# Optimization experiments

Measured on AMD Instinct MI355X. Metric: run time of the kernel, lower is better.

Reference implementation:

```python
import jax, jax.numpy as jnp
import numpy as np
import math

B, S, H, HKV, DH = 2, 2048, 32, 1, 128  # batch, seq, q heads, kv heads, per-head/model dim
D_K = 128


def setup_inputs() -> dict:
    key = jax.random.key(0)
    ks = jax.random.split(key, 11)
    sc = 0.02
    return {
        "query": jax.random.normal(ks[0], (B, S, DH), jnp.float32),
        "key": jax.random.normal(ks[1], (B, S, DH), jnp.float32),
        "values": jax.random.normal(ks[2], (B, S, DH), jnp.float32),
        "W_q": jax.random.normal(ks[3], (DH, H * DH), jnp.float32) * sc,
        "b_q": jnp.zeros((H * DH,), jnp.float32),
        "W_k": jax.random.normal(ks[4], (DH, HKV * DH), jnp.float32) * sc,
        "b_k": jnp.zeros((HKV * DH,), jnp.float32),
        "W_v": jax.random.normal(ks[5], (DH, HKV * DH), jnp.float32) * sc,
        "b_v": jnp.zeros((HKV * DH,), jnp.float32),
        "W_o": jax.random.normal(ks[6], (H * DH, DH), jnp.float32) * sc,
        "b_o": jnp.zeros((DH,), jnp.float32),
    }


def reference(query, key, values, W_q, b_q, W_k, b_k, W_v, b_v, W_o, b_o):
    # Projections (note: the original uses raw .view(-1, H, S, DH), which we
    # replicate exactly — it is a reshape, not a transpose).
    q = (query @ W_q + b_q).reshape(-1, H, S, DH)      # [B,H,S,DH]
    k = (key @ W_k + b_k).reshape(-1, HKV, S, DH)       # [B,1,S,DH]
    v = (values @ W_v + b_v).reshape(-1, HKV, S, DH)    # [B,1,S,DH]

    # RoPE outputs in the original forward are computed but never used
    # (dead code), and mask defaults to None -> no masking. Dropout omitted
    # for deterministic reference.
    scores = jnp.matmul(q, jnp.swapaxes(k, -1, -2)) / math.sqrt(D_K)  # [B,H,S,S]
    attn = jax.nn.softmax(scores, axis=-1)
    out = jnp.matmul(attn, v)                           # [B,H,S,DH]
    out = jnp.swapaxes(out, 1, 2).reshape(-1, S, H * DH)
    return out @ W_o + b_o                              # [B,S,DH]
```

## Files before the change

kernel.cpp:

```cpp
#include <hip/hip_runtime.h>
#include <hip/hip_bf16.h>
#include <math.h>


typedef __hip_bfloat16 bf16;
typedef __attribute__((ext_vector_type(8))) short short8;
typedef __attribute__((ext_vector_type(4))) float floatx4;

static constexpr int B_ = 2;
static constexpr int S_ = 2048;
static constexpr int H_ = 32;
static constexpr int DH_ = 128;

#define GL16(gp, lp)                                              \
  __builtin_amdgcn_global_load_lds(                               \
      (const __attribute__((address_space(1))) void*)(gp),        \
      (__attribute__((address_space(3))) void*)(lp), 16, 0, 0)

static __device__ __forceinline__ bool detect_f32(
    const unsigned short* __restrict__ q) {
  int t = threadIdx.x & 63;
  int cnt = 0;
#pragma unroll
  for (int i = 0; i < 8; ++i) {
    unsigned short u = q[t * 8 + i];
    int e = (u >> 7) & 0xFF;
    if (e < 0x60) cnt++;
  }
#pragma unroll
  for (int off = 1; off < 64; off <<= 1) cnt += __shfl_xor(cnt, off);
  return cnt >= 8;
}

static __device__ void do_ttranspose(const void* __restrict__ W,
                                     bf16* __restrict__ Wt, int K, int N,
                                     bool f, float scale, int bx, int by,
                                     bf16 (*tile)[66]) {
  int n0 = bx * 64, k0 = by * 64;
  int c = threadIdx.x & 63;
  int r4 = threadIdx.x >> 6;
#pragma unroll
  for (int i = 0; i < 16; ++i) {
    int r = r4 * 16 + i;
    float v = f ? ((const float*)W)[(size_t)(k0 + r) * N + n0 + c]
                : __bfloat162float(((const bf16*)W)[(size_t)(k0 + r) * N + n0 + c]);
    tile[r][c] = __float2bfloat16(v * scale);
  }
  __syncthreads();
#pragma unroll
  for (int i = 0; i < 16; ++i) {
    int cc = r4 * 16 + i;
    Wt[(size_t)(n0 + cc) * K + k0 + c] = tile[c][cc];
  }
}

__global__ void prep(const void* __restrict__ query, const void* __restrict__ key,
                     const void* __restrict__ values, bf16* __restrict__ cQ,
                     bf16* __restrict__ cK, bf16* __restrict__ cV,
                     const void* __restrict__ bq, const void* __restrict__ bk,
                     const void* __restrict__ bv, const void* __restrict__ bo,
                     float* __restrict__ fbq, float* __restrict__ fbk,
                     float* __restrict__ fbv, float* __restrict__ fbo,
                     const void* __restrict__ Wq, bf16* __restrict__ Wqt,
                     const void* __restrict__ Wk, bf16* __restrict__ Wkt,
                     const void* __restrict__ Wv, bf16* __restrict__ Wvt,
                     const void* __restrict__ Wo, bf16* __restrict__ Wot,
                     float qscale) {
  __shared__ bf16 tile[64][66];
  const int id = blockIdx.x;
  const bool f = detect_f32((const unsigned short*)query);
  if (id < 6144) {
    int y = id >> 11, x = id & 2047;
    int i = x * 256 + threadIdx.x;
    const void* s = (y == 0) ? query : (y == 1) ? key : values;
    bf16* d = (y == 0) ? cQ : (y == 1) ? cK : cV;
    d[i] = f ? __float2bfloat16(((const float*)s)[i]) : ((const bf16*)s)[i];
  } else if (id < 6162) {
    int i = (id - 6144) * 256 + threadIdx.x;
    const void* s; float* d; int off; float sc = 1.f;
    if (i < 4096) { s = bq; d = fbq; off = i; sc = qscale; }
    else if (i < 4224) { s = bk; d = fbk; off = i - 4096; }
    else if (i < 4352) { s = bv; d = fbv; off = i - 4224; }
    else if (i < 4480) { s = bo; d = fbo; off = i - 4352; }
    else return;
    float v = f ? ((const float*)s)[off]
                : __bfloat162float(((const bf16*)s)[off]);
    d[off] = v * sc;
  } else if (id < 6290) {
    int j = id - 6162;
    do_ttranspose(Wq, Wqt, DH_, H_ * DH_, f, qscale, j % 64, j / 64, tile);
  } else if (id < 6294) {
    int j = id - 6290;
    do_ttranspose(Wk, Wkt, DH_, DH_, f, 1.0f, j % 2, j / 2, tile);
  } else if (id < 6298) {
    int j = id - 6294;
    do_ttranspose(Wv, Wvt, DH_, DH_, f, 1.0f, j % 2, j / 2, tile);
  } else {
    int j = id - 6298;
    do_ttranspose(Wo, Wot, H_ * DH_, DH_, f, 1.0f, j % 2, j / 2, tile);
  }
}

__global__ __launch_bounds__(256) void gemm_qkv(
    const bf16* __restrict__ cQ, const bf16* __restrict__ cK,
    const bf16* __restrict__ cV, const bf16* __restrict__ Wqt,
    const bf16* __restrict__ Wkt, const bf16* __restrict__ Wvt,
    const float* __restrict__ fbq, const float* __restrict__ fbk,
    const float* __restrict__ fbv, bf16* __restrict__ Qp,
    bf16* __restrict__ Kp, bf16* __restrict__ Vtp) {
  const int bx = blockIdx.x;
  const bf16* A; const bf16* Bt; const float* bias; bf16* Cb;
  int mode, ldc, colb;
  if (bx < 64)      { A = cQ; Bt = Wqt; bias = fbq; Cb = Qp;  mode = 0; ldc = 4096; colb = bx; }
  else if (bx < 66) { A = cK; Bt = Wkt; bias = fbk; Cb = Kp;  mode = 0; ldc = 128;  colb = bx - 64; }
  else              { A = cV; Bt = Wvt; bias = fbv; Cb = Vtp; mode = 3; ldc = 0;    colb = bx - 66; }

  const int lane = threadIdx.x & 63;
  const int wave = threadIdx.x >> 6;
  const int lm = lane & 15;
  const int quad = lane >> 4;
  const int row_base = blockIdx.y * 64 + wave * 16;
  const int col_base = colb * 64;

  const bf16* arow = A + (size_t)(row_base + lm) * DH_ + quad * 8;
  const bf16* brow = Bt + (size_t)(col_base + lm) * DH_ + quad * 8;

  floatx4 z = {0.f, 0.f, 0.f, 0.f};
  floatx4 acc[4] = {z, z, z, z};
#pragma unroll
  for (int kk = 0; kk < DH_; kk += 32) {
    short8 a = *(const short8*)(arow + kk);
#pragma unroll
    for (int t = 0; t < 4; ++t) {
      short8 b = *(const short8*)(brow + (size_t)(t * 16) * DH_ + kk);
      acc[t] = __builtin_amdgcn_mfma_f32_16x16x32_bf16(a, b, acc[t], 0, 0, 0);
    }
  }
#pragma unroll
  for (int t = 0; t < 4; ++t) {
    int col = col_base + t * 16 + lm;
#pragma unroll
    for (int r = 0; r < 4; ++r) {
      int row = row_base + quad * 4 + r;
      if (mode == 0) {
        Cb[(size_t)row * ldc + col] = __float2bfloat16(acc[t][r] + bias[col]);
      } else {
        Cb[((size_t)((row >> 11) * DH_ + col)) * S_ + (row & 2047)] =
            __float2bfloat16(acc[t][r] + bias[col]);
      }
    }
  }
}

__global__ __launch_bounds__(256) void gemm_out(
    const bf16* __restrict__ A, const bf16* __restrict__ Bt,
    float* __restrict__ Cf) {
  constexpr int K_len = (H_ * DH_) / 4;
  const int lane = threadIdx.x & 63;
  const int wave = threadIdx.x >> 6;
  const int lm = lane & 15;
  const int quad = lane >> 4;
  const int row_base = blockIdx.y * 64 + wave * 16;
  const int col_base = blockIdx.x * 64;
  const int koff = blockIdx.z * K_len;

  const bf16* arow = A + (size_t)(row_base + lm) * (H_ * DH_) + koff + quad * 8;
  const bf16* brow = Bt + (size_t)(col_base + lm) * (H_ * DH_) + koff + quad * 8;

  floatx4 z = {0.f, 0.f, 0.f, 0.f};
  floatx4 acc[4] = {z, z, z, z};
#pragma unroll 4
  for (int kk = 0; kk < K_len; kk += 32) {
    short8 a = *(const short8*)(arow + kk);
#pragma unroll
    for (int t = 0; t < 4; ++t) {
      short8 b = *(const short8*)(brow + (size_t)(t * 16) * (H_ * DH_) + kk);
      acc[t] = __builtin_amdgcn_mfma_f32_16x16x32_bf16(a, b, acc[t], 0, 0, 0);
    }
  }
#pragma unroll
  for (int t = 0; t < 4; ++t) {
    int col = col_base + t * 16 + lm;
#pragma unroll
    for (int r = 0; r < 4; ++r) {
      int row = row_base + quad * 4 + r;
      Cf[(size_t)blockIdx.z * (4096 * 128) + (size_t)row * DH_ + col] =
          acc[t][r];
    }
  }
}

__global__ void finish_out(const float* __restrict__ parts,
                           const float* __restrict__ bias,
                           float* __restrict__ out) {
  int i = blockIdx.x * 256 + threadIdx.x;
  const float4* p = (const float4*)parts;
  float4 a = p[i];
  float4 b = p[i + 131072];
  float4 c = p[i + 262144];
  float4 d = p[i + 393216];
  float4 bb = ((const float4*)bias)[i & 31];
  float4 o;
  o.x = a.x + b.x + c.x + d.x + bb.x;
  o.y = a.y + b.y + c.y + d.y + bb.y;
  o.z = a.z + b.z + c.z + d.z + bb.z;
  o.w = a.w + b.w + c.w + d.w + bb.w;
  ((float4*)out)[i] = o;
}

static __device__ __forceinline__ unsigned bpack(float lo, float hi) {
  unsigned a = __float_as_uint(lo) + 0x8000u;
  unsigned b = __float_as_uint(hi) + 0x8000u;
  return __builtin_amdgcn_perm(b, a, 0x07060302u);
}

static __device__ __forceinline__ float fexp2(float x) {
#if __has_builtin(__builtin_amdgcn_exp2f)
  return __builtin_amdgcn_exp2f(x);
#else
  return exp2f(x);
#endif
}

static __device__ __forceinline__ void pexchange(const unsigned pk[8],
                                                 int quad, short8* pf) {
  const bool q0 = (quad & 1);
  unsigned sA0 = q0 ? pk[0] : pk[2];
  unsigned sA1 = q0 ? pk[1] : pk[3];
  unsigned sA2 = q0 ? pk[4] : pk[6];
  unsigned sA3 = q0 ? pk[5] : pk[7];
  unsigned r0 = (unsigned)__shfl_xor((int)sA0, 16);
  unsigned r1 = (unsigned)__shfl_xor((int)sA1, 16);
  unsigned r2 = (unsigned)__shfl_xor((int)sA2, 16);
  unsigned r3 = (unsigned)__shfl_xor((int)sA3, 16);
  unsigned M0 = q0 ? r0 : pk[0];
  unsigned M1 = q0 ? r1 : pk[1];
  unsigned M2 = q0 ? pk[2] : r0;
  unsigned M3 = q0 ? pk[3] : r1;
  unsigned M4 = q0 ? r2 : pk[4];
  unsigned M5 = q0 ? r3 : pk[5];
  unsigned M6 = q0 ? pk[6] : r2;
  unsigned M7 = q0 ? pk[7] : r3;
  const bool swp = (quad == 1) || (quad == 2);
  union { unsigned u[4]; short8 v; } f0, f1;
  unsigned t0, t1;
  t0 = (unsigned)__shfl_xor((int)M0, 48); f0.u[0] = swp ? t0 : M0;
  t1 = (unsigned)__shfl_xor((int)M1, 48); f0.u[1] = swp ? t1 : M1;
  t0 = (unsigned)__shfl_xor((int)M2, 48); f0.u[2] = swp ? t0 : M2;
  t1 = (unsigned)__shfl_xor((int)M3, 48); f0.u[3] = swp ? t1 : M3;
  t0 = (unsigned)__shfl_xor((int)M4, 48); f1.u[0] = swp ? t0 : M4;
  t1 = (unsigned)__shfl_xor((int)M5, 48); f1.u[1] = swp ? t1 : M5;
  t0 = (unsigned)__shfl_xor((int)M6, 48); f1.u[2] = swp ? t0 : M6;
  t1 = (unsigned)__shfl_xor((int)M7, 48); f1.u[3] = swp ? t1 : M7;
  pf[0] = f0.v;
  pf[1] = f1.v;
}

__global__ __launch_bounds__(256, 2) void flash_attn(
    const bf16* __restrict__ Qp, const bf16* __restrict__ Kp,
    const bf16* __restrict__ Vt, bf16* __restrict__ O2c) {
  const int tid = threadIdx.x;
  const int lane = tid & 63;
  const int wave = tid >> 6;
  const int lm = lane & 15;
  const int quad = lane >> 4;
  const int qt = blockIdx.x;
  const int h = blockIdx.y;
  const int b = blockIdx.z;

  __shared__ __align__(16) bf16 Klds[64 * 128];
  __shared__ __align__(16) bf16 Vlds[2][128 * 64];

  const int base = qt * 128 + wave * 32;
  const bf16* qrow = Qp + ((size_t)b * S_ + h * 64 + (base >> 5)) * 4096;
  short8 qf0[4], qf1[4];
#pragma unroll
  for (int ks = 0; ks < 4; ++ks) {
    qf0[ks] = *(const short8*)(qrow + lm * 128 + quad * 8 + ks * 32);
    qf1[ks] = *(const short8*)(qrow + (16 + lm) * 128 + quad * 8 + ks * 32);
  }

  const bf16* Kb = Kp + (size_t)b * S_ * DH_;
  const bf16* Vb = Vt + (size_t)b * DH_ * S_;
  const int sw = lm & 7;

  const bf16* kgp[4];
  const bf16* vgp[4];
#pragma unroll
  for (int i = 0; i < 4; ++i) {
    const int inst = wave * 4 + i;
    const int krow = inst * 4 + quad;
    kgp[i] = Kb + (size_t)krow * 128 + ((lm ^ (krow & 7)) * 8);
    const int vrow = inst * 8 + (lane >> 3);
    vgp[i] = Vb + (size_t)vrow * S_ + (((lane & 7) ^ (vrow & 7)) * 8);
  }

  floatx4 z = {0.f, 0.f, 0.f, 0.f};
  floatx4 oa0[8], oa1[8];
#pragma unroll
  for (int nt = 0; nt < 8; ++nt) { oa0[nt] = z; oa1[nt] = z; }
  float ls0 = 0.f, ls1 = 0.f;

#pragma unroll
  for (int i = 0; i < 4; ++i) {
    GL16(kgp[i], &Klds[(wave * 4 + i) * 512]);
    GL16(vgp[i], &Vlds[0][(wave * 4 + i) * 512]);
    kgp[i] += 64 * 128;
    vgp[i] += 64;
  }

  int cur = 0;
  for (int kb = 0; kb < S_; kb += 64) {
    __syncthreads();
    const bool more = kb + 64 < S_;
    if (more) {
#pragma unroll
      for (int i = 0; i < 4; ++i) {
        GL16(vgp[i], &Vlds[cur ^ 1][(wave * 4 + i) * 512]);
        vgp[i] += 64;
      }
    }

    floatx4 s0[4] = {z, z, z, z}, s1[4] = {z, z, z, z};
    __builtin_amdgcn_s_setprio(1);
#pragma unroll
    for (int t = 0; t < 4; ++t) {
#pragma unroll
      for (int ks = 0; ks < 4; ++ks) {
        short8 kf = *(const short8*)(&Klds[(t * 16 + lm) * 128 +
                                           (((quad + 4 * ks) ^ sw) * 8)]);
        s0[t] = __builtin_amdgcn_mfma_f32_16x16x32_bf16(kf, qf0[ks], s0[t],
                                                        0, 0, 0);
        s1[t] = __builtin_amdgcn_mfma_f32_16x16x32_bf16(kf, qf1[ks], s1[t],
                                                        0, 0, 0);
      }
    }
    __builtin_amdgcn_s_setprio(0);

    __syncthreads();
    if (more) {
#pragma unroll
      for (int i = 0; i < 4; ++i) {
        GL16(kgp[i], &Klds[(wave * 4 + i) * 512]);
        kgp[i] += 64 * 128;
      }
    }

    unsigned pk0[8], pk1[8];
#pragma unroll
    for (int t = 0; t < 4; ++t) {
      float a0 = fexp2(s0[t][0]), a1 = fexp2(s0[t][1]);
      float a2 = fexp2(s0[t][2]), a3 = fexp2(s0[t][3]);
      ls0 += (a0 + a1) + (a2 + a3);
      pk0[2 * t] = bpack(a0, a1);
      pk0[2 * t + 1] = bpack(a2, a3);
      float c0 = fexp2(s1[t][0]), c1 = fexp2(s1[t][1]);
      float c2 = fexp2(s1[t][2]), c3 = fexp2(s1[t][3]);
      ls1 += (c0 + c1) + (c2 + c3);
      pk1[2 * t] = bpack(c0, c1);
      pk1[2 * t + 1] = bpack(c2, c3);
    }
    short8 pf0[2], pf1[2];
    pexchange(pk0, quad, pf0);
    pexchange(pk1, quad, pf1);

    __builtin_amdgcn_s_setprio(1);
#pragma unroll
    for (int ks2 = 0; ks2 < 2; ++ks2) {
#pragma unroll
      for (int nt = 0; nt < 8; ++nt) {
        short8 vf = *(const short8*)(&Vlds[cur][(nt * 16 + lm) * 64 +
                                              (((quad + 4 * ks2) ^ sw) * 8)]);
        oa0[nt] = __builtin_amdgcn_mfma_f32_16x16x32_bf16(pf0[ks2], vf,
                                                          oa0[nt], 0, 0, 0);
        oa1[nt] = __builtin_amdgcn_mfma_f32_16x16x32_bf16(pf1[ks2], vf,
                                                          oa1[nt], 0, 0, 0);
      }
    }
    __builtin_amdgcn_s_setprio(0);
    cur ^= 1;
  }

  ls0 += __shfl_xor(ls0, 16);
  ls0 += __shfl_xor(ls0, 32);
  ls1 += __shfl_xor(ls1, 16);
  ls1 += __shfl_xor(ls1, 32);
  float inv0[4], inv1[4];
#pragma unroll
  for (int r = 0; r < 4; ++r) {
    inv0[r] = 1.0f / __shfl(ls0, quad * 4 + r);
    inv1[r] = 1.0f / __shfl(ls1, quad * 4 + r);
  }

#pragma unroll
  for (int r = 0; r < 4; ++r) {
    int s2a = base + quad * 4 + r;
    int s2b = s2a + 16;
    size_t ba = ((size_t)b * S_ + s2a) * 4096 + (size_t)h * 128;
    size_t bb = ((size_t)b * S_ + s2b) * 4096 + (size_t)h * 128;
#pragma unroll
    for (int nt = 0; nt < 8; ++nt) {
      O2c[ba + nt * 16 + lm] = __float2bfloat16(oa0[nt][r] * inv0[r]);
      O2c[bb + nt * 16 + lm] = __float2bfloat16(oa1[nt][r] * inv1[r]);
    }
  }
}

extern "C" void kernel_launch(void* const* d_in, const int* in_sizes, int n_in,
                              void* d_out, int out_size, void* d_ws,
                              size_t ws_size, hipStream_t stream) {
  (void)in_sizes;
  (void)n_in;
  (void)out_size;
  (void)ws_size;

  const void* query = d_in[0];
  const void* key = d_in[1];
  const void* values = d_in[2];
  const void* W_q = d_in[3];
  const void* b_q = d_in[4];
  const void* W_k = d_in[5];
  const void* b_k = d_in[6];
  const void* W_v = d_in[7];
  const void* b_v = d_in[8];
  const void* W_o = d_in[9];
  const void* b_o = d_in[10];
  float* out = (float*)d_out;

  const float kScale = 0.1275174388204085f;
  const int M = B_ * S_;
  const int QN = B_ * S_ * DH_;

  char* w = (char*)d_ws;
  auto carve = [&](size_t bytes) -> char* {
    char* p = w;
    w += (bytes + 255) & ~(size_t)255;
    return p;
  };
  bf16* cQ = (bf16*)carve((size_t)QN * 2);
  bf16* cK = (bf16*)carve((size_t)QN * 2);
  bf16* cV = (bf16*)carve((size_t)QN * 2);
  float* fbq = (float*)carve((size_t)H_ * DH_ * 4);
  float* fbk = (float*)carve((size_t)DH_ * 4);
  float* fbv = (float*)carve((size_t)DH_ * 4);
  float* fbo = (float*)carve((size_t)DH_ * 4);
  bf16* Wqt = (bf16*)carve((size_t)DH_ * H_ * DH_ * 2);
  bf16* Wkt = (bf16*)carve((size_t)DH_ * DH_ * 2);
  bf16* Wvt = (bf16*)carve((size_t)DH_ * DH_ * 2);
  bf16* Wot = (bf16*)carve((size_t)H_ * DH_ * DH_ * 2);
  bf16* Kp = (bf16*)carve((size_t)B_ * S_ * DH_ * 2);
  bf16* Vtp = (bf16*)carve((size_t)B_ * S_ * DH_ * 2);
  bf16* Qp = (bf16*)carve((size_t)M * H_ * DH_ * 2);
  bf16* O2c = (bf16*)carve((size_t)M * H_ * DH_ * 2);

  float* parts = (float*)Qp;

  prep<<<6426, 256, 0, stream>>>(query, key, values, cQ, cK, cV, b_q, b_k,
                                 b_v, b_o, fbq, fbk, fbv, fbo, W_q, Wqt, W_k,
                                 Wkt, W_v, Wvt, W_o, Wot, kScale);

  gemm_qkv<<<dim3(68, 64), 256, 0, stream>>>(cQ, cK, cV, Wqt, Wkt, Wvt, fbq,
                                             fbk, fbv, Qp, Kp, Vtp);

  flash_attn<<<dim3(S_ / 128, H_, B_), 256, 0, stream>>>(Qp, Kp, Vtp, O2c);

  gemm_out<<<dim3(DH_ / 64, M / 64, 4), 256, 0, stream>>>(O2c, Wot, parts);

  finish_out<<<QN / 4 / 256, 256, 0, stream>>>(parts, fbo, out);
}
```

Measured before the change: 319.5 us.

## Fuse input bf16 conversion into QKV GEMM and rebalance output GEMM split-K

Drops the separate pass in prep that converted query/key/values to bf16. The QKV GEMM now reads the raw inputs directly and packs fp32 to bf16 in registers, which removes a full read-write round trip over the activations. Separately, the output GEMM now has each block compute all 128 output columns and splits K eight ways instead of four, with finish_out summing eight partials. This cuts redundant A reads, but it doubles the partial-sum traffic and raises register use per wave.

```diff
diff --git a/kernel.cpp b/kernel.cpp
--- a/kernel.cpp
+++ b/kernel.cpp
@@ -17,6 +17,12 @@
       (const __attribute__((address_space(1))) void*)(gp),        \
       (__attribute__((address_space(3))) void*)(lp), 16, 0, 0)
 
+static __device__ __forceinline__ unsigned bpack(float lo, float hi) {
+  unsigned a = __float_as_uint(lo) + 0x8000u;
+  unsigned b = __float_as_uint(hi) + 0x8000u;
+  return __builtin_amdgcn_perm(b, a, 0x07060302u);
+}
+
 static __device__ __forceinline__ bool detect_f32(
     const unsigned short* __restrict__ q) {
   int t = threadIdx.x & 63;
@@ -30,6 +36,21 @@
 #pragma unroll
   for (int off = 1; off < 64; off <<= 1) cnt += __shfl_xor(cnt, off);
   return cnt >= 8;
+}
+
+static __device__ __forceinline__ short8 loadA8(const void* __restrict__ base,
+                                                size_t elt, bool f) {
+  if (f) {
+    const float4* p = (const float4*)((const float*)base + elt);
+    float4 x = p[0], y = p[1];
+    union { unsigned u[4]; short8 v; } r;
+    r.u[0] = bpack(x.x, x.y);
+    r.u[1] = bpack(x.z, x.w);
+    r.u[2] = bpack(y.x, y.y);
+    r.u[3] = bpack(y.z, y.w);
+    return r.v;
+  }
+  return *(const short8*)((const bf16*)base + elt);
 }
 
 static __device__ void do_ttranspose(const void* __restrict__ W,
@@ -54,9 +75,7 @@
   }
 }
 
-__global__ void prep(const void* __restrict__ query, const void* __restrict__ key,
-                     const void* __restrict__ values, bf16* __restrict__ cQ,
-                     bf16* __restrict__ cK, bf16* __restrict__ cV,
+__global__ void prep(const void* __restrict__ query,
                      const void* __restrict__ bq, const void* __restrict__ bk,
                      const void* __restrict__ bv, const void* __restrict__ bo,
                      float* __restrict__ fbq, float* __restrict__ fbk,
@@ -69,14 +88,8 @@
   __shared__ bf16 tile[64][66];
   const int id = blockIdx.x;
   const bool f = detect_f32((const unsigned short*)query);
-  if (id < 6144) {
-    int y = id >> 11, x = id & 2047;
-    int i = x * 256 + threadIdx.x;
-    const void* s = (y == 0) ? query : (y == 1) ? key : values;
-    bf16* d = (y == 0) ? cQ : (y == 1) ? cK : cV;
-    d[i] = f ? __float2bfloat16(((const float*)s)[i]) : ((const bf16*)s)[i];
-  } else if (id < 6162) {
-    int i = (id - 6144) * 256 + threadIdx.x;
+  if (id < 18) {
+    int i = id * 256 + threadIdx.x;
     const void* s; float* d; int off; float sc = 1.f;
     if (i < 4096) { s = bq; d = fbq; off = i; sc = qscale; }
     else if (i < 4224) { s = bk; d = fbk; off = i - 4096; }
@@ -86,35 +99,36 @@
     float v = f ? ((const float*)s)[off]
                 : __bfloat162float(((const bf16*)s)[off]);
     d[off] = v * sc;
-  } else if (id < 6290) {
-    int j = id - 6162;
+  } else if (id < 146) {
+    int j = id - 18;
     do_ttranspose(Wq, Wqt, DH_, H_ * DH_, f, qscale, j % 64, j / 64, tile);
-  } else if (id < 6294) {
-    int j = id - 6290;
+  } else if (id < 150) {
+    int j = id - 146;
     do_ttranspose(Wk, Wkt, DH_, DH_, f, 1.0f, j % 2, j / 2, tile);
-  } else if (id < 6298) {
-    int j = id - 6294;
+  } else if (id < 154) {
+    int j = id - 150;
     do_ttranspose(Wv, Wvt, DH_, DH_, f, 1.0f, j % 2, j / 2, tile);
   } else {
-    int j = id - 6298;
+    int j = id - 154;
     do_ttranspose(Wo, Wot, H_ * DH_, DH_, f, 1.0f, j % 2, j / 2, tile);
   }
 }
 
 __global__ __launch_bounds__(256) void gemm_qkv(
-    const bf16* __restrict__ cQ, const bf16* __restrict__ cK,
-    const bf16* __restrict__ cV, const bf16* __restrict__ Wqt,
+    const void* __restrict__ query, const void* __restrict__ key,
+    const void* __restrict__ values, const bf16* __restrict__ Wqt,
     const bf16* __restrict__ Wkt, const bf16* __restrict__ Wvt,
     const float* __restrict__ fbq, const float* __restrict__ fbk,
     const float* __restrict__ fbv, bf16* __restrict__ Qp,
     bf16* __restrict__ Kp, bf16* __restrict__ Vtp) {
   const int bx = blockIdx.x;
-  const bf16* A; const bf16* Bt; const float* bias; bf16* Cb;
+  const void* A; const bf16* Bt; const float* bias; bf16* Cb;
   int mode, ldc, colb;
-  if (bx < 64)      { A = cQ; Bt = Wqt; bias = fbq; Cb = Qp;  mode = 0; ldc = 4096; colb = bx; }
-  else if (bx < 66) { A = cK; Bt = Wkt; bias = fbk; Cb = Kp;  mode = 0; ldc = 128;  colb = bx - 64; }
-  else              { A = cV; Bt = Wvt; bias = fbv; Cb = Vtp; mode = 3; ldc = 0;    colb = bx - 66; }
-
+  if (bx < 64)      { A = query;  Bt = Wqt; bias = fbq; Cb = Qp;  mode = 0; ldc = 4096; colb = bx; }
+  else if (bx < 66) { A = key;    Bt = Wkt; bias = fbk; Cb = Kp;  mode = 0; ldc = 128;  colb = bx - 64; }
+  else              { A = values; Bt = Wvt; bias = fbv; Cb = Vtp; mode = 3; ldc = 0;    colb = bx - 66; }
+
+  const bool f = detect_f32((const unsigned short*)query);
   const int lane = threadIdx.x & 63;
   const int wave = threadIdx.x >> 6;
   const int lm = lane & 15;
@@ -122,14 +136,14 @@
   const int row_base = blockIdx.y * 64 + wave * 16;
   const int col_base = colb * 64;
 
-  const bf16* arow = A + (size_t)(row_base + lm) * DH_ + quad * 8;
+  const size_t aelt = (size_t)(row_base + lm) * DH_ + quad * 8;
   const bf16* brow = Bt + (size_t)(col_base + lm) * DH_ + quad * 8;
 
   floatx4 z = {0.f, 0.f, 0.f, 0.f};
   floatx4 acc[4] = {z, z, z, z};
 #pragma unroll
   for (int kk = 0; kk < DH_; kk += 32) {
-    short8 a = *(const short8*)(arow + kk);
+    short8 a = loadA8(A, aelt + kk, f);
 #pragma unroll
     for (int t = 0; t < 4; ++t) {
       short8 b = *(const short8*)(brow + (size_t)(t * 16) * DH_ + kk);
@@ -155,36 +169,35 @@
 __global__ __launch_bounds__(256) void gemm_out(
     const bf16* __restrict__ A, const bf16* __restrict__ Bt,
     float* __restrict__ Cf) {
-  constexpr int K_len = (H_ * DH_) / 4;
+  constexpr int K_len = (H_ * DH_) / 8;
   const int lane = threadIdx.x & 63;
   const int wave = threadIdx.x >> 6;
   const int lm = lane & 15;
   const int quad = lane >> 4;
-  const int row_base = blockIdx.y * 64 + wave * 16;
-  const int col_base = blockIdx.x * 64;
-  const int koff = blockIdx.z * K_len;
+  const int row_base = blockIdx.x * 64 + wave * 16;
+  const int koff = blockIdx.y * K_len;
 
   const bf16* arow = A + (size_t)(row_base + lm) * (H_ * DH_) + koff + quad * 8;
-  const bf16* brow = Bt + (size_t)(col_base + lm) * (H_ * DH_) + koff + quad * 8;
+  const bf16* brow = Bt + (size_t)lm * (H_ * DH_) + koff + quad * 8;
 
   floatx4 z = {0.f, 0.f, 0.f, 0.f};
-  floatx4 acc[4] = {z, z, z, z};
-#pragma unroll 4
+  floatx4 acc[8] = {z, z, z, z, z, z, z, z};
+#pragma unroll 2
   for (int kk = 0; kk < K_len; kk += 32) {
     short8 a = *(const short8*)(arow + kk);
 #pragma unroll
-    for (int t = 0; t < 4; ++t) {
+    for (int t = 0; t < 8; ++t) {
       short8 b = *(const short8*)(brow + (size_t)(t * 16) * (H_ * DH_) + kk);
       acc[t] = __builtin_amdgcn_mfma_f32_16x16x32_bf16(a, b, acc[t], 0, 0, 0);
     }
   }
 #pragma unroll
-  for (int t = 0; t < 4; ++t) {
-    int col = col_base + t * 16 + lm;
+  for (int t = 0; t < 8; ++t) {
+    int col = t * 16 + lm;
 #pragma unroll
     for (int r = 0; r < 4; ++r) {
       int row = row_base + quad * 4 + r;
-      Cf[(size_t)blockIdx.z * (4096 * 128) + (size_t)row * DH_ + col] =
+      Cf[(size_t)blockIdx.y * (4096 * 128) + (size_t)row * DH_ + col] =
           acc[t][r];
     }
   }
@@ -195,23 +208,14 @@
                            float* __restrict__ out) {
   int i = blockIdx.x * 256 + threadIdx.x;
   const float4* p = (const float4*)parts;
-  float4 a = p[i];
-  float4 b = p[i + 131072];
-  float4 c = p[i + 262144];
-  float4 d = p[i + 393216];
   float4 bb = ((const float4*)bias)[i & 31];
-  float4 o;
-  o.x = a.x + b.x + c.x + d.x + bb.x;
-  o.y = a.y + b.y + c.y + d.y + bb.y;
-  o.z = a.z + b.z + c.z + d.z + bb.z;
-  o.w = a.w + b.w + c.w + d.w + bb.w;
+  float4 o = bb;
+#pragma unroll
+  for (int j = 0; j < 8; ++j) {
+    float4 a = p[i + (size_t)j * 131072];
+    o.x += a.x; o.y += a.y; o.z += a.z; o.w += a.w;
+  }
   ((float4*)out)[i] = o;
-}
-
-static __device__ __forceinline__ unsigned bpack(float lo, float hi) {
-  unsigned a = __float_as_uint(lo) + 0x8000u;
-  unsigned b = __float_as_uint(hi) + 0x8000u;
-  return __builtin_amdgcn_perm(b, a, 0x07060302u);
 }
 
 static __device__ __forceinline__ float fexp2(float x) {
@@ -437,9 +441,6 @@
     w += (bytes + 255) & ~(size_t)255;
     return p;
   };
-  bf16* cQ = (bf16*)carve((size_t)QN * 2);
-  bf16* cK = (bf16*)carve((size_t)QN * 2);
-  bf16* cV = (bf16*)carve((size_t)QN * 2);
   float* fbq = (float*)carve((size_t)H_ * DH_ * 4);
   float* fbk = (float*)carve((size_t)DH_ * 4);
   float* fbv = (float*)carve((size_t)DH_ * 4);
@@ -455,16 +456,16 @@
 
   float* parts = (float*)Qp;
 
-  prep<<<6426, 256, 0, stream>>>(query, key, values, cQ, cK, cV, b_q, b_k,
-                                 b_v, b_o, fbq, fbk, fbv, fbo, W_q, Wqt, W_k,
-                                 Wkt, W_v, Wvt, W_o, Wot, kScale);
-
-  gemm_qkv<<<dim3(68, 64), 256, 0, stream>>>(cQ, cK, cV, Wqt, Wkt, Wvt, fbq,
-                                             fbk, fbv, Qp, Kp, Vtp);
+  prep<<<282, 256, 0, stream>>>(query, b_q, b_k, b_v, b_o, fbq, fbk, fbv,
+                                fbo, W_q, Wqt, W_k, Wkt, W_v, Wvt, W_o, Wot,
+                                kScale);
+
+  gemm_qkv<<<dim3(68, 64), 256, 0, stream>>>(query, key, values, Wqt, Wkt,
+                                             Wvt, fbq, fbk, fbv, Qp, Kp, Vtp);
 
   flash_attn<<<dim3(S_ / 128, H_, B_), 256, 0, stream>>>(Qp, Kp, Vtp, O2c);
 
-  gemm_out<<<dim3(DH_ / 64, M / 64, 4), 256, 0, stream>>>(O2c, Wot, parts);
+  gemm_out<<<dim3(M / 64, 8), 256, 0, stream>>>(O2c, Wot, parts);
 
   finish_out<<<QN / 4 / 256, 256, 0, stream>>>(parts, fbo, out);
 }
```

Result: no change. 324.8 us (+1.7%).
